# Optimization experiments

Hardware: AMD Instinct MI355X
Metric: run time of the kernel (lower is better)

The kernel has to match this reference:

```python
import jax, jax.numpy as jnp
import numpy as np

TEMPERATURE = 0.5


def setup_inputs() -> dict:
    key = jax.random.key(0)
    k1, k2 = jax.random.split(key)
    z_i = jax.random.normal(k1, (4096, 512), dtype=jnp.float32)
    z_j = jax.random.normal(k2, (4096, 512), dtype=jnp.float32)
    return {"z_i": z_i, "z_j": z_j}


def reference(z_i, z_j):
    B = z_i.shape[0]
    # L2-normalize embeddings (cosine sim of normalized vecs == dot product)
    zi = z_i / jnp.linalg.norm(z_i, axis=1, keepdims=True)
    zj = z_j / jnp.linalg.norm(z_j, axis=1, keepdims=True)
    p = jnp.concatenate([zi, zj], axis=0)                      # [2B, D]
    sim = jnp.matmul(p, p.T) / TEMPERATURE                     # [2B, 2B]
    # positives: sim(i, i+B) and sim(i+B, i)
    pos = jnp.concatenate([jnp.diagonal(sim, offset=B),
                           jnp.diagonal(sim, offset=-B)])      # [2B]
    # CE with label 0 over [pos, negatives]: logsumexp covers pos + negatives,
    # i.e. all row entries except the self-similarity diagonal.
    n = 2 * B
    neg_inf = jnp.finfo(sim.dtype).min
    sim_masked = jnp.where(jnp.eye(n, dtype=bool), neg_inf, sim)
    lse = jax.nn.logsumexp(sim_masked, axis=1)                 # [2B]
    loss = jnp.sum(lse - pos) / n
    return loss
```

## Files before the change

kernel.cpp:

```cpp
#include <hip/hip_runtime.h>
#include <hip/hip_bf16.h>
#include <stdint.h>

#define NB    4096
#define NROWS 8192
#define DIM   512
#define BM    128
#define ROWB  256
#define SBLK  512
#define NREP  8

typedef __attribute__((ext_vector_type(4))) float f32x4;
typedef __attribute__((ext_vector_type(4))) int   i32x4;
typedef __attribute__((ext_vector_type(8))) int   i32x8;

#define SCALE_E8M0 0x7A7A7A7Au

__device__ __forceinline__ uint32_t f2e2m1(float x) {
  uint32_t s = (__float_as_uint(x) >> 28) & 0x8u;
  float a = fabsf(x);
  uint32_t m =
      (a <= 0.25f) ? 0u :
      (a <  0.75f) ? 1u :
      (a <= 1.25f) ? 2u :
      (a <  1.75f) ? 3u :
      (a <= 2.50f) ? 4u :
      (a <  3.50f) ? 5u :
      (a <= 5.00f) ? 6u : 7u;
  return s | m;
}

__device__ __forceinline__ void gload_lds16(const void* g, void* l) {
  __builtin_amdgcn_global_load_lds(
      (const __attribute__((address_space(1))) void*)g,
      (__attribute__((address_space(3))) void*)l, 16, 0, 0);
}

__device__ __forceinline__ i32x8 pad8(i32x4 v) {
  i32x8 r = {v[0], v[1], v[2], v[3], 0, 0, 0, 0};
  return r;
}

__global__ __launch_bounds__(256) void normalize_pos_kernel(
    const float* __restrict__ zi, const float* __restrict__ zj,
    unsigned char* __restrict__ p, float* __restrict__ rowsum,
    float* __restrict__ posp) {
  __shared__ float ws4[4];
  const int wave = threadIdx.x >> 6;
  const int lane = threadIdx.x & 63;
  const int i    = blockIdx.x * 4 + wave;

  int gt = blockIdx.x * 256 + threadIdx.x;
  if (gt < NREP * NROWS) rowsum[gt] = 0.f;

  const float4* sa = (const float4*)(zi + (size_t)i * DIM);
  const float4* sb = (const float4*)(zj + (size_t)i * DIM);
  float4 a0 = sa[lane * 2], a1 = sa[lane * 2 + 1];
  float4 b0 = sb[lane * 2], b1 = sb[lane * 2 + 1];
  float va[8] = {a0.x, a0.y, a0.z, a0.w, a1.x, a1.y, a1.z, a1.w};
  float vb[8] = {b0.x, b0.y, b0.z, b0.w, b1.x, b1.y, b1.z, b1.w};
  float ssa = 0.f, ssb = 0.f;
#pragma unroll
  for (int j = 0; j < 8; ++j) { ssa += va[j] * va[j]; ssb += vb[j] * vb[j]; }
#pragma unroll
  for (int off = 32; off; off >>= 1) {
    ssa += __shfl_xor(ssa, off);
    ssb += __shfl_xor(ssb, off);
  }
  float inva = rsqrtf(ssa), invb = rsqrtf(ssb);

  uint32_t pa = 0, pb = 0;
  float d = 0.f;
#pragma unroll
  for (int j = 0; j < 8; ++j) {
    float na = va[j] * inva, nb = vb[j] * invb;
    pa |= f2e2m1(na * 32.0f) << (4 * j);
    pb |= f2e2m1(nb * 32.0f) << (4 * j);
    d += na * nb;
  }
  *(uint32_t*)(p + (size_t)i * ROWB + lane * 4)        = pa;
  *(uint32_t*)(p + (size_t)(i + NB) * ROWB + lane * 4) = pb;

#pragma unroll
  for (int off = 32; off; off >>= 1) d += __shfl_xor(d, off);
  if (lane == 0) ws4[wave] = d;
  __syncthreads();
  if (threadIdx.x == 0)
    posp[blockIdx.x] = 4.0f * (ws4[0] + ws4[1] + ws4[2] + ws4[3]);
}

__device__ __forceinline__ void decode_tile(int x, int l, int* pbi, int* pbj) {
  if (x < 6) {
    const int sqi[6] = {0, 0, 0, 1, 1, 2};
    const int sqj[6] = {1, 2, 3, 2, 3, 3};
    *pbi = sqi[x] * 16 + (l >> 4);
    *pbj = sqj[x] * 16 + (l & 15);
  } else {
    int s  = (x == 6) ? 0 : 2;
    int ll = l;
    if (ll >= 136) { ll -= 136; s += 1; }
    int i = 0;
    while ((i + 1) * (33 - (i + 1)) / 2 <= ll) ++i;
    int j = i + (ll - i * (33 - i) / 2);
    *pbi = s * 16 + i;
    *pbj = s * 16 + j;
  }
}

__global__ __launch_bounds__(256, 2) void simexp_kernel(
    const unsigned char* __restrict__ p, float* __restrict__ rowsum) {
  __shared__ __align__(16) unsigned char As[BM * ROWB];
  __shared__ __align__(16) unsigned char Bs[BM * ROWB];

  const int x  = blockIdx.x & 7;
  const int lb = blockIdx.x >> 3;
  int start, cnt;
  if (x < 6) { start = lb * 4; cnt = 4; }
  else if (lb < 48) { start = lb * 4; cnt = 4; }
  else { start = 192 + (lb - 48) * 5; cnt = 5; }

  float* __restrict__ rs = rowsum + (size_t)x * NROWS;

  const int tid  = threadIdx.x;
  const int wave = tid >> 6;
  const int lane = tid & 63;
  const int wm   = wave >> 1;
  const int wn   = wave & 1;
  const int frow = lane & 15;
  const int kc   = lane >> 4;

  const int row4 = lane >> 4;
  const int ch   = lane & 15;

#define STAGE_PANEL(dst_, rowbase_)                                           \
  {                                                                           \
    _Pragma("unroll")                                                         \
    for (int q = 0; q < 8; ++q) {                                             \
      int rbase = wave * 32 + q * 4;                                          \
      int gch   = ch ^ ((rbase + row4) & 15);                                 \
      gload_lds16(p + (size_t)((rowbase_) + rbase + row4) * ROWB + gch * 16,  \
                  (char*)(dst_) + rbase * ROWB);                              \
    }                                                                         \
  }

  const int r4 = lane >> 4;
  const int cl = lane & 15;

  int pbi = -1;
  for (int tt = 0; tt < cnt; ++tt) {
    int cbi, cbj;
    decode_tile(x, start + tt, &cbi, &cbj);
    const bool diag = (cbi == cbj);

    if (cbi != pbi) STAGE_PANEL(As, cbi * BM);
    STAGE_PANEL(Bs, cbj * BM);
    pbi = cbi;
    __syncthreads();

    f32x4 acc[4][4] = {};
#pragma unroll
    for (int t = 0; t < 4; ++t) {
      const int coft = (((t * 4 + kc) ^ frow) * 16);
      i32x8 af[4], bfr[4];
#pragma unroll
      for (int m = 0; m < 4; ++m)
        af[m] = pad8(*(const i32x4*)(
            As + (wm * 64 + m * 16 + frow) * ROWB + coft));
#pragma unroll
      for (int n = 0; n < 4; ++n)
        bfr[n] = pad8(*(const i32x4*)(
            Bs + (wn * 64 + n * 16 + frow) * ROWB + coft));
#pragma unroll
      for (int m = 0; m < 4; ++m)
#pragma unroll
        for (int n = 0; n < 4; ++n)
          acc[m][n] = __builtin_amdgcn_mfma_scale_f32_16x16x128_f8f6f4(
              af[m], bfr[n], acc[m][n], 4 , 4 ,
              0, SCALE_E8M0, 0, SCALE_E8M0);
    }

    float rowpart[4][4];
    float colpart[4] = {0.f, 0.f, 0.f, 0.f};

    if (diag) {
#pragma unroll
      for (int m = 0; m < 4; ++m)
#pragma unroll
        for (int r = 0; r < 4; ++r) {
          int grow = cbi * BM + wm * 64 + m * 16 + r4 * 4 + r;
          float s = 0.f;
#pragma unroll
          for (int n = 0; n < 4; ++n) {
            int gcol = cbj * BM + wn * 64 + n * 16 + cl;
            float e  = __expf(2.0f * acc[m][n][r]);
            s += (grow == gcol) ? 0.f : e;
          }
          rowpart[m][r] = s;
        }
    } else {
#pragma unroll
      for (int m = 0; m < 4; ++m)
#pragma unroll
        for (int r = 0; r < 4; ++r) {
          float s = 0.f;
#pragma unroll
          for (int n = 0; n < 4; ++n) {
            float e = __expf(2.0f * acc[m][n][r]);
            s += e;
            colpart[n] += e;
          }
          rowpart[m][r] = s;
        }
    }

#pragma unroll
    for (int m = 0; m < 4; ++m)
#pragma unroll
      for (int r = 0; r < 4; ++r) {
        float s = rowpart[m][r];
        s += __shfl_xor(s, 1);
        s += __shfl_xor(s, 2);
        s += __shfl_xor(s, 4);
        s += __shfl_xor(s, 8);
        if (cl == 0) {
          int grow = cbi * BM + wm * 64 + m * 16 + r4 * 4 + r;
          atomicAdd(&rs[grow], s);
        }
      }

    if (!diag) {
#pragma unroll
      for (int n = 0; n < 4; ++n) {
        float c = colpart[n];
        c += __shfl_xor(c, 16);
        c += __shfl_xor(c, 32);
        if (r4 == 0) {
          int gcol = cbj * BM + wn * 64 + n * 16 + cl;
          atomicAdd(&rs[gcol], c);
        }
      }
    }

    __syncthreads();
  }
}

__global__ __launch_bounds__(256) void finalize1_kernel(
    const float* __restrict__ rowsum, const float* __restrict__ posp,
    float* __restrict__ part) {
  __shared__ float ws4[4];
  const int b   = blockIdx.x;
  const int tid = threadIdx.x;
  float v = 0.f;
  if (tid < 128) {
    int row = b * 128 + tid;
    float s = 0.f;
#pragma unroll
    for (int r = 0; r < NREP; ++r) s += rowsum[r * NROWS + row];
    v += logf(s);
  } else if (tid < 144) {
    v -= posp[b * 16 + (tid - 128)];
  }
#pragma unroll
  for (int off = 32; off; off >>= 1) v += __shfl_xor(v, off);
  if ((tid & 63) == 0) ws4[tid >> 6] = v;
  __syncthreads();
  if (tid == 0) part[b] = ws4[0] + ws4[1] + ws4[2] + ws4[3];
}

__global__ __launch_bounds__(64) void finalize2_kernel(
    const float* __restrict__ part, float* __restrict__ out) {
  int tid = threadIdx.x;
  float v = part[tid];
#pragma unroll
  for (int off = 32; off; off >>= 1) v += __shfl_xor(v, off);
  if (tid == 0) out[0] = v / (float)NROWS;
}

extern "C" void kernel_launch(void* const* d_in, const int* in_sizes, int n_in,
                              void* d_out, int out_size, void* d_ws,
                              size_t ws_size, hipStream_t stream) {
  const float* zi = (const float*)d_in[0];
  const float* zj = (const float*)d_in[1];
  float* out      = (float*)d_out;

  char* ws          = (char*)d_ws;
  unsigned char* p  = (unsigned char*)ws;
  float* rowsum     = (float*)(ws + (size_t)NROWS * ROWB);
  float* posp       = rowsum + NREP * NROWS;
  float* part       = posp + 1024;

  normalize_pos_kernel<<<1024, 256, 0, stream>>>(zi, zj, p, rowsum, posp);
  simexp_kernel<<<SBLK, 256, 0, stream>>>(p, rowsum);
  finalize1_kernel<<<64, 256, 0, stream>>>(rowsum, posp, part);
  finalize2_kernel<<<1, 64, 0, stream>>>(part, out);
}
```

Baseline: 42.68 us.

## Prefetch next tile panels during epilogue and merge finalize kernels

The sim-exp loop now issues the loads for the next tile's A/B panels into LDS right after the MFMA loop, so they overlap the exp/reduction epilogue instead of stalling at the start of each tile. A single barrier before staging guards against overwriting panels still being read. The two finalize kernels are merged into one single-block kernel, saving a launch but doing the 8192-row reduction serially in one block.

```diff
diff --git a/kernel.cpp b/kernel.cpp
--- a/kernel.cpp
+++ b/kernel.cpp
@@ -146,16 +146,14 @@
   const int r4 = lane >> 4;
   const int cl = lane & 15;
 
-  int pbi = -1;
+  int cbi, cbj;
+  decode_tile(x, start, &cbi, &cbj);
+  STAGE_PANEL(As, cbi * BM);
+  STAGE_PANEL(Bs, cbj * BM);
+  __syncthreads();
+
   for (int tt = 0; tt < cnt; ++tt) {
-    int cbi, cbj;
-    decode_tile(x, start + tt, &cbi, &cbj);
     const bool diag = (cbi == cbj);
-
-    if (cbi != pbi) STAGE_PANEL(As, cbi * BM);
-    STAGE_PANEL(Bs, cbj * BM);
-    pbi = cbi;
-    __syncthreads();
 
     f32x4 acc[4][4] = {};
 #pragma unroll
@@ -177,6 +175,15 @@
           acc[m][n] = __builtin_amdgcn_mfma_scale_f32_16x16x128_f8f6f4(
               af[m], bfr[n], acc[m][n], 4 , 4 ,
               0, SCALE_E8M0, 0, SCALE_E8M0);
+    }
+
+    const bool more = (tt + 1 < cnt);
+    int nbi = cbi, nbj = cbj;
+    if (more) decode_tile(x, start + tt + 1, &nbi, &nbj);
+    __syncthreads();
+    if (more) {
+      if (nbi != cbi) STAGE_PANEL(As, nbi * BM);
+      STAGE_PANEL(Bs, nbj * BM);
     }
 
     float rowpart[4][4];
@@ -241,40 +248,30 @@
       }
     }
 
-    __syncthreads();
-  }
-}
-
-__global__ __launch_bounds__(256) void finalize1_kernel(
+    if (more) __syncthreads();
+    cbi = nbi; cbj = nbj;
+  }
+}
+
+__global__ __launch_bounds__(256) void finalize_kernel(
     const float* __restrict__ rowsum, const float* __restrict__ posp,
-    float* __restrict__ part) {
+    float* __restrict__ out) {
   __shared__ float ws4[4];
-  const int b   = blockIdx.x;
   const int tid = threadIdx.x;
   float v = 0.f;
-  if (tid < 128) {
-    int row = b * 128 + tid;
+  for (int row = tid; row < NROWS; row += 256) {
     float s = 0.f;
 #pragma unroll
     for (int r = 0; r < NREP; ++r) s += rowsum[r * NROWS + row];
     v += logf(s);
-  } else if (tid < 144) {
-    v -= posp[b * 16 + (tid - 128)];
-  }
+  }
+  for (int i = tid; i < 1024; i += 256) v -= posp[i];
 #pragma unroll
   for (int off = 32; off; off >>= 1) v += __shfl_xor(v, off);
   if ((tid & 63) == 0) ws4[tid >> 6] = v;
   __syncthreads();
-  if (tid == 0) part[b] = ws4[0] + ws4[1] + ws4[2] + ws4[3];
-}
-
-__global__ __launch_bounds__(64) void finalize2_kernel(
-    const float* __restrict__ part, float* __restrict__ out) {
-  int tid = threadIdx.x;
-  float v = part[tid];
-#pragma unroll
-  for (int off = 32; off; off >>= 1) v += __shfl_xor(v, off);
-  if (tid == 0) out[0] = v / (float)NROWS;
+  if (tid == 0)
+    out[0] = (ws4[0] + ws4[1] + ws4[2] + ws4[3]) / (float)NROWS;
 }
 
 extern "C" void kernel_launch(void* const* d_in, const int* in_sizes, int n_in,
@@ -290,8 +287,8 @@
   float* posp       = rowsum + NREP * NROWS;
   float* part       = posp + 1024;
 
+  (void)part;
   normalize_pos_kernel<<<1024, 256, 0, stream>>>(zi, zj, p, rowsum, posp);
   simexp_kernel<<<SBLK, 256, 0, stream>>>(p, rowsum);
-  finalize1_kernel<<<64, 256, 0, stream>>>(rowsum, posp, part);
-  finalize2_kernel<<<1, 64, 0, stream>>>(part, out);
-}
+  finalize_kernel<<<1, 256, 0, stream>>>(rowsum, posp, out);
+}
```

Result: slower. 67.44 us (+58.0%).

## Fuse normalize and similarity kernels with a grid-wide atomic barrier

Applied to the files above, without the earlier changes.

Merges the normalization/quantization kernel into the similarity-exp kernel. Each of the 512 blocks first normalizes 8 rows, then all blocks wait at a global atomic-counter barrier before running the MXFP4 tile work. This removes one kernel launch and its gap. It adds a hipMemsetAsync for the counter and relies on all 512 blocks being co-resident (2 per CU), otherwise the barrier would deadlock. The posp indexing in finalize is adjusted to 8 rows per block.

```diff
diff --git a/kernel.cpp b/kernel.cpp
--- a/kernel.cpp
+++ b/kernel.cpp
@@ -39,54 +39,6 @@
 __device__ __forceinline__ i32x8 pad8(i32x4 v) {
   i32x8 r = {v[0], v[1], v[2], v[3], 0, 0, 0, 0};
   return r;
-}
-
-__global__ __launch_bounds__(256) void normalize_pos_kernel(
-    const float* __restrict__ zi, const float* __restrict__ zj,
-    unsigned char* __restrict__ p, float* __restrict__ rowsum,
-    float* __restrict__ posp) {
-  __shared__ float ws4[4];
-  const int wave = threadIdx.x >> 6;
-  const int lane = threadIdx.x & 63;
-  const int i    = blockIdx.x * 4 + wave;
-
-  int gt = blockIdx.x * 256 + threadIdx.x;
-  if (gt < NREP * NROWS) rowsum[gt] = 0.f;
-
-  const float4* sa = (const float4*)(zi + (size_t)i * DIM);
-  const float4* sb = (const float4*)(zj + (size_t)i * DIM);
-  float4 a0 = sa[lane * 2], a1 = sa[lane * 2 + 1];
-  float4 b0 = sb[lane * 2], b1 = sb[lane * 2 + 1];
-  float va[8] = {a0.x, a0.y, a0.z, a0.w, a1.x, a1.y, a1.z, a1.w};
-  float vb[8] = {b0.x, b0.y, b0.z, b0.w, b1.x, b1.y, b1.z, b1.w};
-  float ssa = 0.f, ssb = 0.f;
-#pragma unroll
-  for (int j = 0; j < 8; ++j) { ssa += va[j] * va[j]; ssb += vb[j] * vb[j]; }
-#pragma unroll
-  for (int off = 32; off; off >>= 1) {
-    ssa += __shfl_xor(ssa, off);
-    ssb += __shfl_xor(ssb, off);
-  }
-  float inva = rsqrtf(ssa), invb = rsqrtf(ssb);
-
-  uint32_t pa = 0, pb = 0;
-  float d = 0.f;
-#pragma unroll
-  for (int j = 0; j < 8; ++j) {
-    float na = va[j] * inva, nb = vb[j] * invb;
-    pa |= f2e2m1(na * 32.0f) << (4 * j);
-    pb |= f2e2m1(nb * 32.0f) << (4 * j);
-    d += na * nb;
-  }
-  *(uint32_t*)(p + (size_t)i * ROWB + lane * 4)        = pa;
-  *(uint32_t*)(p + (size_t)(i + NB) * ROWB + lane * 4) = pb;
-
-#pragma unroll
-  for (int off = 32; off; off >>= 1) d += __shfl_xor(d, off);
-  if (lane == 0) ws4[wave] = d;
-  __syncthreads();
-  if (threadIdx.x == 0)
-    posp[blockIdx.x] = 4.0f * (ws4[0] + ws4[1] + ws4[2] + ws4[3]);
 }
 
 __device__ __forceinline__ void decode_tile(int x, int l, int* pbi, int* pbj) {
@@ -107,13 +59,74 @@
   }
 }
 
-__global__ __launch_bounds__(256, 2) void simexp_kernel(
-    const unsigned char* __restrict__ p, float* __restrict__ rowsum) {
+__global__ __launch_bounds__(256, 2) void fused_kernel(
+    const float* __restrict__ zi, const float* __restrict__ zj,
+    unsigned char* __restrict__ p, float* __restrict__ rowsum,
+    float* __restrict__ posp, int* __restrict__ ctr) {
   __shared__ __align__(16) unsigned char As[BM * ROWB];
   __shared__ __align__(16) unsigned char Bs[BM * ROWB];
-
-  const int x  = blockIdx.x & 7;
-  const int lb = blockIdx.x >> 3;
+  __shared__ float ws4[4];
+
+  const int bid  = blockIdx.x;
+  const int tid  = threadIdx.x;
+  const int wave = tid >> 6;
+  const int lane = tid & 63;
+
+  {
+    int g = bid * 256 + tid;
+    if (g < NREP * NROWS) rowsum[g] = 0.f;
+
+    float dtot = 0.f;
+#pragma unroll
+    for (int it = 0; it < 2; ++it) {
+      const int i = bid * 8 + it * 4 + wave;
+      const float4* sa = (const float4*)(zi + (size_t)i * DIM);
+      const float4* sb = (const float4*)(zj + (size_t)i * DIM);
+      float4 a0 = sa[lane * 2], a1 = sa[lane * 2 + 1];
+      float4 b0 = sb[lane * 2], b1 = sb[lane * 2 + 1];
+      float va[8] = {a0.x, a0.y, a0.z, a0.w, a1.x, a1.y, a1.z, a1.w};
+      float vb[8] = {b0.x, b0.y, b0.z, b0.w, b1.x, b1.y, b1.z, b1.w};
+      float ssa = 0.f, ssb = 0.f;
+#pragma unroll
+      for (int j = 0; j < 8; ++j) { ssa += va[j] * va[j]; ssb += vb[j] * vb[j]; }
+#pragma unroll
+      for (int off = 32; off; off >>= 1) {
+        ssa += __shfl_xor(ssa, off);
+        ssb += __shfl_xor(ssb, off);
+      }
+      float inva = rsqrtf(ssa), invb = rsqrtf(ssb);
+      uint32_t pa = 0, pb = 0;
+#pragma unroll
+      for (int j = 0; j < 8; ++j) {
+        float na = va[j] * inva, nb = vb[j] * invb;
+        pa |= f2e2m1(na * 32.0f) << (4 * j);
+        pb |= f2e2m1(nb * 32.0f) << (4 * j);
+        dtot += na * nb;
+      }
+      *(uint32_t*)(p + (size_t)i * ROWB + lane * 4)        = pa;
+      *(uint32_t*)(p + (size_t)(i + NB) * ROWB + lane * 4) = pb;
+    }
+#pragma unroll
+    for (int off = 32; off; off >>= 1) dtot += __shfl_xor(dtot, off);
+    if (lane == 0) ws4[wave] = dtot;
+    __syncthreads();
+    if (tid == 0)
+      posp[bid] = 4.0f * (ws4[0] + ws4[1] + ws4[2] + ws4[3]);
+  }
+
+  __threadfence();
+  __syncthreads();
+  if (tid == 0) {
+    __hip_atomic_fetch_add(ctr, 1, __ATOMIC_ACQ_REL, __HIP_MEMORY_SCOPE_AGENT);
+    while (__hip_atomic_load(ctr, __ATOMIC_ACQUIRE,
+                             __HIP_MEMORY_SCOPE_AGENT) < SBLK)
+      __builtin_amdgcn_s_sleep(16);
+  }
+  __syncthreads();
+  __threadfence();
+
+  const int x  = bid & 7;
+  const int lb = bid >> 3;
   int start, cnt;
   if (x < 6) { start = lb * 4; cnt = 4; }
   else if (lb < 48) { start = lb * 4; cnt = 4; }
@@ -121,9 +134,6 @@
 
   float* __restrict__ rs = rowsum + (size_t)x * NROWS;
 
-  const int tid  = threadIdx.x;
-  const int wave = tid >> 6;
-  const int lane = tid & 63;
   const int wm   = wave >> 1;
   const int wn   = wave & 1;
   const int frow = lane & 15;
@@ -258,8 +268,8 @@
 #pragma unroll
     for (int r = 0; r < NREP; ++r) s += rowsum[r * NROWS + row];
     v += logf(s);
-  } else if (tid < 144) {
-    v -= posp[b * 16 + (tid - 128)];
+  } else if (tid < 136) {
+    v -= posp[b * 8 + (tid - 128)];
   }
 #pragma unroll
   for (int off = 32; off; off >>= 1) v += __shfl_xor(v, off);
@@ -288,10 +298,11 @@
   unsigned char* p  = (unsigned char*)ws;
   float* rowsum     = (float*)(ws + (size_t)NROWS * ROWB);
   float* posp       = rowsum + NREP * NROWS;
-  float* part       = posp + 1024;
-
-  normalize_pos_kernel<<<1024, 256, 0, stream>>>(zi, zj, p, rowsum, posp);
-  simexp_kernel<<<SBLK, 256, 0, stream>>>(p, rowsum);
+  float* part       = posp + SBLK;
+  int*   ctr        = (int*)(part + 64);
+
+  hipMemsetAsync(ctr, 0, sizeof(int), stream);
+  fused_kernel<<<SBLK, 256, 0, stream>>>(zi, zj, p, rowsum, posp, ctr);
   finalize1_kernel<<<64, 256, 0, stream>>>(rowsum, posp, part);
   finalize2_kernel<<<1, 64, 0, stream>>>(part, out);
 }
```

Result: slower. 132.3 us (+210.1%).
